# Kernel tuning notes

Measured on AMD Instinct MI355X. Metric: run time of the kernel, lower is better.

The kernel has to match this reference:

```python
import jax, jax.numpy as jnp
import numpy as np

B, S, D, H, DFF = 4, 2048, 1024, 16, 4096
DK = D // H
EPS = 1e-6


def setup_inputs() -> dict:
    key = jax.random.key(0)
    ks = jax.random.split(key, 8)
    s = 0.02
    return {
        "x": jax.random.normal(ks[0], (B, S, D), jnp.float32),
        "src_mask": jnp.ones((B, 1, 1, S), jnp.int32),
        "w_q": jax.random.normal(ks[1], (D, D), jnp.float32) * s,
        "w_k": jax.random.normal(ks[2], (D, D), jnp.float32) * s,
        "w_v": jax.random.normal(ks[3], (D, D), jnp.float32) * s,
        "w_o": jax.random.normal(ks[4], (D, D), jnp.float32) * s,
        "w1": jax.random.normal(ks[5], (DFF, D), jnp.float32) * s,
        "b1": jnp.zeros((DFF,), jnp.float32),
        "w2": jax.random.normal(ks[6], (D, DFF), jnp.float32) * s,
        "b2": jnp.zeros((D,), jnp.float32),
        "gamma1": jnp.ones((1,), jnp.float32),
        "beta1": jnp.zeros((1,), jnp.float32),
        "gamma2": jnp.ones((1,), jnp.float32),
        "beta2": jnp.zeros((1,), jnp.float32),
    }


def layernorm(x, gamma, beta):
    # matches torch source: unbiased std (ddof=1), eps added to std, scalar gamma/beta
    mean = jnp.mean(x, axis=-1, keepdims=True)
    std = jnp.std(x, axis=-1, keepdims=True, ddof=1)
    return gamma * (x - mean) / (std + EPS) + beta


def mha(x, w_q, w_k, w_v, w_o):
    # Linear(bias=False): y = x @ W.T
    q = (x @ w_q.T).reshape(B, S, H, DK).transpose(0, 2, 1, 3)  # [B,H,S,DK]
    k = (x @ w_k.T).reshape(B, S, H, DK).transpose(0, 2, 1, 3)
    v = (x @ w_v.T).reshape(B, S, H, DK).transpose(0, 2, 1, 3)
    scores = jnp.einsum('bhqd,bhkd->bhqk', q, k) / np.float32(np.sqrt(DK))
    # NOTE: source calls attention.masked_fill(...) without assigning the result,
    # so the mask has no effect; faithfully replicated (mask unused).
    attn = jax.nn.softmax(scores, axis=-1)
    ctx = jnp.einsum('bhqk,bhkd->bhqd', attn, v)  # [B,H,S,DK]
    ctx = ctx.transpose(0, 2, 1, 3).reshape(B, S, D)
    return ctx @ w_o.T


def ffn(x, w1, b1, w2, b2):
    return jax.nn.relu(x @ w1.T + b1) @ w2.T + b2


def reference(x, src_mask, w_q, w_k, w_v, w_o, w1, b1, w2, b2,
              gamma1, beta1, gamma2, beta2):
    # pre-norm residual blocks; dropout is identity in eval
    x = x + mha(layernorm(x, gamma1, beta1), w_q, w_k, w_v, w_o)
    x = x + ffn(layernorm(x, gamma2, beta2), w1, b1, w2, b2)
    return x
```

## Files before the change

kernel.cpp:

```cpp
#include <hip/hip_runtime.h>
#include <hip/hip_bf16.h>

#define DEV static __device__ __forceinline__

typedef unsigned short u16;
typedef float fp32x4 __attribute__((ext_vector_type(4)));
typedef short bf16x8 __attribute__((ext_vector_type(8)));
typedef short bf16x4 __attribute__((ext_vector_type(4)));

DEV float bf2f(u16 u) { return __uint_as_float(((unsigned)u) << 16); }
DEV u16 f2bf(float f) {
  unsigned x = __float_as_uint(f);
  x += 0x7fffu + ((x >> 16) & 1u);
  return (u16)(x >> 16);
}

DEV void gload_lds16(const void* g, void* l) {
  __builtin_amdgcn_global_load_lds(
      (__attribute__((address_space(1))) void*)(unsigned long long)g,
      (__attribute__((address_space(3))) void*)(unsigned int)(unsigned long long)l,
      16, 0, 0);
}

__global__ __launch_bounds__(256) void cvt_kernel(const float* __restrict__ in,
                                                  u16* __restrict__ out) {
  const int i = blockIdx.x * 256 + threadIdx.x;
  const fp32x4 v = ((const fp32x4*)in)[i];
  bf16x4 o;
#pragma unroll
  for (int j = 0; j < 4; j++) o[j] = (short)f2bf(v[j]);
  ((bf16x4*)out)[i] = o;
}

__global__ __launch_bounds__(256) void ln_kernel(const float* __restrict__ x,
                                                 u16* __restrict__ y,
                                                 const float* __restrict__ gamma,
                                                 const float* __restrict__ beta) {
  const int row = blockIdx.x;
  const int t = threadIdx.x;
  const fp32x4 v = ((const fp32x4*)(x + (size_t)row * 1024))[t];
  float s = v[0] + v[1] + v[2] + v[3];
  float ss = v[0] * v[0] + v[1] * v[1] + v[2] * v[2] + v[3] * v[3];
#pragma unroll
  for (int o = 32; o > 0; o >>= 1) {
    s += __shfl_down(s, o);
    ss += __shfl_down(ss, o);
  }
  __shared__ float rs[4], rss[4];
  const int w = t >> 6;
  if ((t & 63) == 0) { rs[w] = s; rss[w] = ss; }
  __syncthreads();
  const float S = rs[0] + rs[1] + rs[2] + rs[3];
  const float SS = rss[0] + rss[1] + rss[2] + rss[3];
  const float mean = S * (1.0f / 1024.0f);
  const float var = fmaxf((SS - 1024.0f * mean * mean) * (1.0f / 1023.0f), 0.0f);
  const float sc = gamma[0] / (sqrtf(var) + 1e-6f);
  const float be = beta[0];
  bf16x4 o;
#pragma unroll
  for (int j = 0; j < 4; j++) o[j] = (short)f2bf((v[j] - mean) * sc + be);
  ((bf16x4*)(y + (size_t)row * 1024))[t] = o;
}

template <int EPI>
__global__ __launch_bounds__(256, 2) void gemm_bt(
    const u16* __restrict__ A, const u16* __restrict__ W, u16* __restrict__ Cb,
    float* __restrict__ Cf, const float* __restrict__ bias,
    const float* __restrict__ resid, int M, int N, int K) {
  __shared__ u16 sA[128 * 32];
  __shared__ u16 sB[128 * 32];
  const int t = threadIdx.x;
  const int lane = t & 63;
  const int w = t >> 6;
  const int wr = (w >> 1) * 64;
  const int wc = (w & 1) * 64;
  const int lr = lane & 15;
  const int hi = lane >> 4;
  const int bx = blockIdx.x, by = blockIdx.y;

  const u16* gA = A + (size_t)(by * 128 + (t >> 2)) * K + (t & 3) * 8;
  const u16* gB = W + (size_t)(bx * 128 + (t >> 2)) * K + (t & 3) * 8;
  const size_t rstep = (size_t)64 * K;
  u16* lA = &sA[t * 8];
  u16* lB = &sB[t * 8];

  const fp32x4 zero4 = {0.f, 0.f, 0.f, 0.f};
  fp32x4 acc[4][4];
#pragma unroll
  for (int i = 0; i < 4; i++)
#pragma unroll
    for (int j = 0; j < 4; j++) acc[i][j] = zero4;

  for (int k0 = 0; k0 < K; k0 += 32) {
    gload_lds16(gA, lA);
    gload_lds16(gA + rstep, lA + 2048);
    gload_lds16(gB, lB);
    gload_lds16(gB + rstep, lB + 2048);
    gA += 32;
    gB += 32;
    __syncthreads();
    bf16x8 af[4], bfr[4];
#pragma unroll
    for (int i = 0; i < 4; i++)
      af[i] = *(const bf16x8*)&sA[(wr + i * 16 + lr) * 32 + hi * 8];
#pragma unroll
    for (int j = 0; j < 4; j++)
      bfr[j] = *(const bf16x8*)&sB[(wc + j * 16 + lr) * 32 + hi * 8];
#pragma unroll
    for (int i = 0; i < 4; i++)
#pragma unroll
      for (int j = 0; j < 4; j++)
        acc[i][j] =
            __builtin_amdgcn_mfma_f32_16x16x32_bf16(af[i], bfr[j], acc[i][j], 0, 0, 0);
    __syncthreads();
  }

  const int row0 = by * 128 + wr + hi * 4;
  const int col0 = bx * 128 + wc + lr;
  float bj[4] = {0.f, 0.f, 0.f, 0.f};
  if (EPI == 1 || EPI == 3) {
#pragma unroll
    for (int j = 0; j < 4; j++) bj[j] = bias[col0 + j * 16];
  }
#pragma unroll
  for (int i = 0; i < 4; i++) {
#pragma unroll
    for (int r = 0; r < 4; r++) {
      const size_t row = (size_t)(row0 + i * 16 + r);
#pragma unroll
      for (int j = 0; j < 4; j++) {
        const int col = col0 + j * 16;
        float v = acc[i][j][r];
        if (EPI == 1) v = fmaxf(v + bj[j], 0.f);
        if (EPI == 3) v += bj[j];
        if (EPI >= 2) {
          v += resid[row * N + col];
          Cf[row * N + col] = v;
        } else {
          Cb[row * N + col] = f2bf(v);
        }
      }
    }
  }
}

__global__ __launch_bounds__(256) void vtrans_kernel(const u16* __restrict__ V,
                                                     u16* __restrict__ VT) {
  const int st = blockIdx.x;
  const int h = blockIdx.y;
  const int b = blockIdx.z;
  const int t = threadIdx.x;
  const int r = t >> 2, c0 = (t & 3) * 16;
  __shared__ u16 sT[64][72];

  const u16* src = V + ((size_t)(b * 2048 + st * 64 + r)) * 1024 + h * 64 + c0;
  bf16x8 v0 = *(const bf16x8*)src;
  bf16x8 v1 = *(const bf16x8*)(src + 8);
  const int cb = c0 ^ ((r >> 4) << 4);
  *(bf16x8*)&sT[r][cb] = v0;
  *(bf16x8*)&sT[r][cb + 8] = v1;
  __syncthreads();

  const int dc = r ^ ((c0 >> 4) << 4);
  bf16x8 o0, o1;
#pragma unroll
  for (int i = 0; i < 8; i++) o0[i] = sT[c0 + i][dc];
#pragma unroll
  for (int i = 0; i < 8; i++) o1[i] = sT[c0 + 8 + i][dc];
  u16* dst = VT + ((size_t)((b * 16 + h) * 64 + r)) * 2048 + st * 64 + c0;
  *(bf16x8*)dst = o0;
  *(bf16x8*)(dst + 8) = o1;
}

__global__ __launch_bounds__(256, 2) void attn_kernel(const u16* __restrict__ Q,
                                                      const u16* __restrict__ K,
                                                      const u16* __restrict__ VT,
                                                      u16* __restrict__ O) {
  const int qt = blockIdx.x;
  const int h = blockIdx.y;
  const int b = blockIdx.z;
  const int t = threadIdx.x, lane = t & 63, w = t >> 6;
  const int lr = lane & 15, hi = lane >> 4;

  __shared__ u16 sK[64][72];
  __shared__ u16 sVT[64][72];
  __shared__ u16 sQP[64][72];

  const size_t base = ((size_t)b * 2048) * 1024 + (size_t)h * 64;
  const size_t vbase = (((size_t)b * 16 + h) * 64) * 2048;
  const int r = t >> 2, c0 = (t & 3) * 16;

  {
    const u16* src = Q + base + (size_t)(qt * 64 + r) * 1024 + c0;
    bf16x8 u0 = *(const bf16x8*)src;
    bf16x8 u1 = *(const bf16x8*)(src + 8);
#pragma unroll
    for (int i = 0; i < 8; i++) sQP[r][c0 + i] = f2bf(bf2f((u16)u0[i]) * 0.125f);
#pragma unroll
    for (int i = 0; i < 8; i++) sQP[r][c0 + 8 + i] = f2bf(bf2f((u16)u1[i]) * 0.125f);
  }
  __syncthreads();
  bf16x8 qreg0 = *(const bf16x8*)&sQP[w * 16 + lr][hi * 8];
  bf16x8 qreg1 = *(const bf16x8*)&sQP[w * 16 + lr][32 + hi * 8];

  bf16x8 kA, kB, vA, vB;
  {
    const u16* ks = K + base + (size_t)r * 1024 + c0;
    kA = *(const bf16x8*)ks;
    kB = *(const bf16x8*)(ks + 8);
    const u16* vs = VT + vbase + (size_t)r * 2048 + c0;
    vA = *(const bf16x8*)vs;
    vB = *(const bf16x8*)(vs + 8);
  }

  const fp32x4 zero4 = {0.f, 0.f, 0.f, 0.f};
  fp32x4 onT[4];
#pragma unroll
  for (int df = 0; df < 4; df++) onT[df] = zero4;
  float mrun = -1e30f, lrun = 0.f;

  for (int kt = 0; kt < 32; ++kt) {
    __syncthreads();
    *(bf16x8*)&sK[r][c0] = kA;
    *(bf16x8*)&sK[r][c0 + 8] = kB;
    *(bf16x8*)&sVT[r][c0] = vA;
    *(bf16x8*)&sVT[r][c0 + 8] = vB;
    __syncthreads();
    if (kt < 31) {
      const u16* kn = K + base + (size_t)((kt + 1) * 64 + r) * 1024 + c0;
      kA = *(const bf16x8*)kn;
      kB = *(const bf16x8*)(kn + 8);
      const u16* vn = VT + vbase + (size_t)r * 2048 + (kt + 1) * 64 + c0;
      vA = *(const bf16x8*)vn;
      vB = *(const bf16x8*)(vn + 8);
    }

    fp32x4 sc[4];
#pragma unroll
    for (int kk = 0; kk < 4; kk++) {
      fp32x4 a = zero4;
      bf16x8 kf0 = *(const bf16x8*)&sK[kk * 16 + lr][hi * 8];
      bf16x8 kf1 = *(const bf16x8*)&sK[kk * 16 + lr][32 + hi * 8];
      a = __builtin_amdgcn_mfma_f32_16x16x32_bf16(kf0, qreg0, a, 0, 0, 0);
      a = __builtin_amdgcn_mfma_f32_16x16x32_bf16(kf1, qreg1, a, 0, 0, 0);
      sc[kk] = a;
    }

    float mloc = -1e30f;
#pragma unroll
    for (int kk = 0; kk < 4; kk++)
#pragma unroll
      for (int rr = 0; rr < 4; rr++) mloc = fmaxf(mloc, sc[kk][rr]);
    mloc = fmaxf(mloc, __shfl_xor(mloc, 16));
    mloc = fmaxf(mloc, __shfl_xor(mloc, 32));
    const float mnew = fmaxf(mrun, mloc);
    const float alpha = __expf(mrun - mnew);
    float psum = 0.f;
#pragma unroll
    for (int kk = 0; kk < 4; kk++) {
      bf16x4 pv;
#pragma unroll
      for (int rr = 0; rr < 4; rr++) {
        const float p = __expf(sc[kk][rr] - mnew);
        psum += p;
        pv[rr] = (short)f2bf(p);
      }
      *(bf16x4*)&sQP[w * 16 + lr][kk * 16 + hi * 4] = pv;
    }
    psum += __shfl_xor(psum, 16);
    psum += __shfl_xor(psum, 32);
    lrun = lrun * alpha + psum;
    mrun = mnew;
#pragma unroll
    for (int df = 0; df < 4; df++) onT[df] *= alpha;

#pragma unroll
    for (int df = 0; df < 4; df++) {
#pragma unroll
      for (int ks = 0; ks < 2; ks++) {
        bf16x8 vf = *(const bf16x8*)&sVT[df * 16 + lr][ks * 32 + hi * 8];
        bf16x8 pf = *(const bf16x8*)&sQP[w * 16 + lr][ks * 32 + hi * 8];
        onT[df] = __builtin_amdgcn_mfma_f32_16x16x32_bf16(vf, pf, onT[df], 0, 0, 0);
      }
    }
  }

  const float invl = 1.0f / lrun;
  u16* dst = O + base + (size_t)(qt * 64 + w * 16 + lr) * 1024;
#pragma unroll
  for (int df = 0; df < 4; df++) {
    bf16x4 o4;
#pragma unroll
    for (int rr = 0; rr < 4; rr++) o4[rr] = (short)f2bf(onT[df][rr] * invl);
    *(bf16x4*)&dst[df * 16 + hi * 4] = o4;
  }
}

extern "C" void kernel_launch(void* const* d_in, const int* in_sizes, int n_in,
                              void* d_out, int out_size, void* d_ws, size_t ws_size,
                              hipStream_t stream) {
  const float* x = (const float*)d_in[0];
  const float* wq = (const float*)d_in[2];
  const float* wk = (const float*)d_in[3];
  const float* wv = (const float*)d_in[4];
  const float* wo = (const float*)d_in[5];
  const float* w1 = (const float*)d_in[6];
  const float* b1 = (const float*)d_in[7];
  const float* w2 = (const float*)d_in[8];
  const float* b2 = (const float*)d_in[9];
  const float* g1 = (const float*)d_in[10];
  const float* be1 = (const float*)d_in[11];
  const float* g2 = (const float*)d_in[12];
  const float* be2 = (const float*)d_in[13];
  float* out = (float*)d_out;

  const size_t MB = 1024ull * 1024ull;
  char* ws = (char*)d_ws;
  if (ws_size < 136 * MB) return;

  u16* wqb = (u16*)(ws + 0 * MB);
  u16* wkb = (u16*)(ws + 2 * MB);
  u16* wvb = (u16*)(ws + 4 * MB);
  u16* wob = (u16*)(ws + 6 * MB);
  u16* w1b = (u16*)(ws + 8 * MB);
  u16* w2b = (u16*)(ws + 16 * MB);
  u16* Qb = (u16*)(ws + 24 * MB);
  u16* Kb = (u16*)(ws + 40 * MB);
  u16* Vb = (u16*)(ws + 56 * MB);
  u16* Ctx = (u16*)(ws + 72 * MB);
  u16* Hb = (u16*)(ws + 24 * MB);
  u16* Yb = (u16*)(ws + 88 * MB);
  u16* VTb = (u16*)(ws + 88 * MB);
  float* X2 = (float*)(ws + 104 * MB);

  dim3 blk(256);

  cvt_kernel<<<1024, blk, 0, stream>>>(wq, wqb);
  cvt_kernel<<<1024, blk, 0, stream>>>(wk, wkb);
  cvt_kernel<<<1024, blk, 0, stream>>>(wv, wvb);
  cvt_kernel<<<1024, blk, 0, stream>>>(wo, wob);
  cvt_kernel<<<4096, blk, 0, stream>>>(w1, w1b);
  cvt_kernel<<<4096, blk, 0, stream>>>(w2, w2b);

  ln_kernel<<<8192, blk, 0, stream>>>(x, Yb, g1, be1);

  gemm_bt<0><<<dim3(8, 64), blk, 0, stream>>>(Yb, wqb, Qb, nullptr, nullptr, nullptr,
                                              8192, 1024, 1024);
  gemm_bt<0><<<dim3(8, 64), blk, 0, stream>>>(Yb, wkb, Kb, nullptr, nullptr, nullptr,
                                              8192, 1024, 1024);
  gemm_bt<0><<<dim3(8, 64), blk, 0, stream>>>(Yb, wvb, Vb, nullptr, nullptr, nullptr,
                                              8192, 1024, 1024);
  vtrans_kernel<<<dim3(32, 16, 4), blk, 0, stream>>>(Vb, VTb);

  attn_kernel<<<dim3(32, 16, 4), blk, 0, stream>>>(Qb, Kb, VTb, Ctx);

  gemm_bt<2><<<dim3(8, 64), blk, 0, stream>>>(Ctx, wob, nullptr, X2, nullptr, x, 8192,
                                              1024, 1024);

  ln_kernel<<<8192, blk, 0, stream>>>(X2, Yb, g2, be2);

  gemm_bt<1><<<dim3(32, 64), blk, 0, stream>>>(Yb, w1b, Hb, nullptr, b1, nullptr, 8192,
                                               4096, 1024);

  gemm_bt<3><<<dim3(8, 64), blk, 0, stream>>>(Hb, w2b, nullptr, out, b2, X2, 8192, 1024,
                                              4096);
}
```

Baseline: 499.7 us.

## Enlarge attention block to 128 queries with XOR-swizzled LDS and exp2 softmax

The attention kernel now runs 512 threads per block over 128 query rows, so each staged K/V tile is shared by twice as many query rows and K/V global traffic drops by half. Shared-memory indexing uses an XOR swizzle to avoid bank conflicts. The log2(e) factor is folded into the Q scale so softmax can use exp2f. Bf16 packing goes through v_cvt_pk_bf16_f32 instead of manual rounding. Launch bounds of (512, 8) may constrain registers, and the larger blocks halve the grid size.

```diff
diff --git a/kernel.cpp b/kernel.cpp
--- a/kernel.cpp
+++ b/kernel.cpp
@@ -13,6 +13,12 @@
   unsigned x = __float_as_uint(f);
   x += 0x7fffu + ((x >> 16) & 1u);
   return (u16)(x >> 16);
+}
+
+DEV unsigned cvt_pk_bf16(float a, float b) {
+  unsigned r;
+  asm("v_cvt_pk_bf16_f32 %0, %1, %2" : "=v"(r) : "v"(a), "v"(b));
+  return r;
 }
 
 DEV void gload_lds16(const void* g, void* l) {
@@ -172,7 +178,12 @@
   *(bf16x8*)(dst + 8) = o1;
 }
 
-__global__ __launch_bounds__(256, 2) void attn_kernel(const u16* __restrict__ Q,
+DEV u16* lp(u16* rowp, int row, int col) {
+  const int ch = col >> 3, sub = col & 7;
+  return rowp + (((ch ^ (row & 7)) << 3) + sub);
+}
+
+__global__ __launch_bounds__(512, 8) void attn_kernel(const u16* __restrict__ Q,
                                                       const u16* __restrict__ K,
                                                       const u16* __restrict__ VT,
                                                       u16* __restrict__ O) {
@@ -184,34 +195,36 @@
 
   __shared__ u16 sK[64][72];
   __shared__ u16 sVT[64][72];
-  __shared__ u16 sQP[64][72];
+  __shared__ u16 sQP[128][72];
 
   const size_t base = ((size_t)b * 2048) * 1024 + (size_t)h * 64;
   const size_t vbase = (((size_t)b * 16 + h) * 64) * 2048;
-  const int r = t >> 2, c0 = (t & 3) * 16;
 
   {
-    const u16* src = Q + base + (size_t)(qt * 64 + r) * 1024 + c0;
+    const int r = t >> 2, c0 = (t & 3) * 16;
+    const float qs = 0.125f * 1.44269504f;
+    const u16* src = Q + base + (size_t)(qt * 128 + r) * 1024 + c0;
     bf16x8 u0 = *(const bf16x8*)src;
     bf16x8 u1 = *(const bf16x8*)(src + 8);
-#pragma unroll
-    for (int i = 0; i < 8; i++) sQP[r][c0 + i] = f2bf(bf2f((u16)u0[i]) * 0.125f);
-#pragma unroll
-    for (int i = 0; i < 8; i++) sQP[r][c0 + 8 + i] = f2bf(bf2f((u16)u1[i]) * 0.125f);
+    union { unsigned u[4]; bf16x8 v; } q0, q1;
+#pragma unroll
+    for (int j = 0; j < 4; j++)
+      q0.u[j] = cvt_pk_bf16(bf2f((u16)u0[2 * j]) * qs, bf2f((u16)u0[2 * j + 1]) * qs);
+#pragma unroll
+    for (int j = 0; j < 4; j++)
+      q1.u[j] = cvt_pk_bf16(bf2f((u16)u1[2 * j]) * qs, bf2f((u16)u1[2 * j + 1]) * qs);
+    *(bf16x8*)lp(sQP[r], r, c0) = q0.v;
+    *(bf16x8*)lp(sQP[r], r, c0 + 8) = q1.v;
   }
   __syncthreads();
-  bf16x8 qreg0 = *(const bf16x8*)&sQP[w * 16 + lr][hi * 8];
-  bf16x8 qreg1 = *(const bf16x8*)&sQP[w * 16 + lr][32 + hi * 8];
-
-  bf16x8 kA, kB, vA, vB;
-  {
-    const u16* ks = K + base + (size_t)r * 1024 + c0;
-    kA = *(const bf16x8*)ks;
-    kB = *(const bf16x8*)(ks + 8);
-    const u16* vs = VT + vbase + (size_t)r * 2048 + c0;
-    vA = *(const bf16x8*)vs;
-    vB = *(const bf16x8*)(vs + 8);
-  }
+  const int qrow = w * 16 + lr;
+  bf16x8 qreg0 = *(const bf16x8*)lp(sQP[qrow], qrow, hi * 8);
+  bf16x8 qreg1 = *(const bf16x8*)lp(sQP[qrow], qrow, 32 + hi * 8);
+
+  const int rk = t >> 3, ck = (t & 7) * 8;
+  bf16x8 kA, vA;
+  kA = *(const bf16x8*)(K + base + (size_t)rk * 1024 + ck);
+  vA = *(const bf16x8*)(VT + vbase + (size_t)rk * 2048 + ck);
 
   const fp32x4 zero4 = {0.f, 0.f, 0.f, 0.f};
   fp32x4 onT[4];
@@ -221,26 +234,21 @@
 
   for (int kt = 0; kt < 32; ++kt) {
     __syncthreads();
-    *(bf16x8*)&sK[r][c0] = kA;
-    *(bf16x8*)&sK[r][c0 + 8] = kB;
-    *(bf16x8*)&sVT[r][c0] = vA;
-    *(bf16x8*)&sVT[r][c0 + 8] = vB;
+    *(bf16x8*)lp(sK[rk], rk, ck) = kA;
+    *(bf16x8*)lp(sVT[rk], rk, ck) = vA;
     __syncthreads();
     if (kt < 31) {
-      const u16* kn = K + base + (size_t)((kt + 1) * 64 + r) * 1024 + c0;
-      kA = *(const bf16x8*)kn;
-      kB = *(const bf16x8*)(kn + 8);
-      const u16* vn = VT + vbase + (size_t)r * 2048 + (kt + 1) * 64 + c0;
-      vA = *(const bf16x8*)vn;
-      vB = *(const bf16x8*)(vn + 8);
+      kA = *(const bf16x8*)(K + base + (size_t)((kt + 1) * 64 + rk) * 1024 + ck);
+      vA = *(const bf16x8*)(VT + vbase + (size_t)rk * 2048 + (kt + 1) * 64 + ck);
     }
 
     fp32x4 sc[4];
 #pragma unroll
     for (int kk = 0; kk < 4; kk++) {
       fp32x4 a = zero4;
-      bf16x8 kf0 = *(const bf16x8*)&sK[kk * 16 + lr][hi * 8];
-      bf16x8 kf1 = *(const bf16x8*)&sK[kk * 16 + lr][32 + hi * 8];
+      const int krow = kk * 16 + lr;
+      bf16x8 kf0 = *(const bf16x8*)lp(sK[krow], krow, hi * 8);
+      bf16x8 kf1 = *(const bf16x8*)lp(sK[krow], krow, 32 + hi * 8);
       a = __builtin_amdgcn_mfma_f32_16x16x32_bf16(kf0, qreg0, a, 0, 0, 0);
       a = __builtin_amdgcn_mfma_f32_16x16x32_bf16(kf1, qreg1, a, 0, 0, 0);
       sc[kk] = a;
@@ -254,18 +262,15 @@
     mloc = fmaxf(mloc, __shfl_xor(mloc, 16));
     mloc = fmaxf(mloc, __shfl_xor(mloc, 32));
     const float mnew = fmaxf(mrun, mloc);
-    const float alpha = __expf(mrun - mnew);
+    const float alpha = exp2f(mrun - mnew);
     float psum = 0.f;
 #pragma unroll
     for (int kk = 0; kk < 4; kk++) {
-      bf16x4 pv;
-#pragma unroll
-      for (int rr = 0; rr < 4; rr++) {
-        const float p = __expf(sc[kk][rr] - mnew);
-        psum += p;
-        pv[rr] = (short)f2bf(p);
-      }
-      *(bf16x4*)&sQP[w * 16 + lr][kk * 16 + hi * 4] = pv;
+      float p0 = exp2f(sc[kk][0] - mnew), p1 = exp2f(sc[kk][1] - mnew);
+      float p2 = exp2f(sc[kk][2] - mnew), p3 = exp2f(sc[kk][3] - mnew);
+      psum += (p0 + p1) + (p2 + p3);
+      uint2 pk = {cvt_pk_bf16(p0, p1), cvt_pk_bf16(p2, p3)};
+      *(uint2*)lp(sQP[qrow], qrow, kk * 16 + hi * 4) = pk;
     }
     psum += __shfl_xor(psum, 16);
     psum += __shfl_xor(psum, 32);
@@ -276,23 +281,23 @@
 
 #pragma unroll
     for (int df = 0; df < 4; df++) {
+      const int vrow = df * 16 + lr;
 #pragma unroll
       for (int ks = 0; ks < 2; ks++) {
-        bf16x8 vf = *(const bf16x8*)&sVT[df * 16 + lr][ks * 32 + hi * 8];
-        bf16x8 pf = *(const bf16x8*)&sQP[w * 16 + lr][ks * 32 + hi * 8];
+        bf16x8 vf = *(const bf16x8*)lp(sVT[vrow], vrow, ks * 32 + hi * 8);
+        bf16x8 pf = *(const bf16x8*)lp(sQP[qrow], qrow, ks * 32 + hi * 8);
         onT[df] = __builtin_amdgcn_mfma_f32_16x16x32_bf16(vf, pf, onT[df], 0, 0, 0);
       }
     }
   }
 
   const float invl = 1.0f / lrun;
-  u16* dst = O + base + (size_t)(qt * 64 + w * 16 + lr) * 1024;
+  u16* dst = O + base + (size_t)(qt * 128 + qrow) * 1024;
 #pragma unroll
   for (int df = 0; df < 4; df++) {
-    bf16x4 o4;
-#pragma unroll
-    for (int rr = 0; rr < 4; rr++) o4[rr] = (short)f2bf(onT[df][rr] * invl);
-    *(bf16x4*)&dst[df * 16 + hi * 4] = o4;
+    uint2 o2 = {cvt_pk_bf16(onT[df][0] * invl, onT[df][1] * invl),
+                cvt_pk_bf16(onT[df][2] * invl, onT[df][3] * invl)};
+    *(uint2*)&dst[df * 16 + hi * 4] = o2;
   }
 }
 
@@ -352,7 +357,7 @@
                                               8192, 1024, 1024);
   vtrans_kernel<<<dim3(32, 16, 4), blk, 0, stream>>>(Vb, VTb);
 
-  attn_kernel<<<dim3(32, 16, 4), blk, 0, stream>>>(Qb, Kb, VTb, Ctx);
+  attn_kernel<<<dim3(16, 16, 4), dim3(512), 0, stream>>>(Qb, Kb, VTb, Ctx);
 
   gemm_bt<2><<<dim3(8, 64), blk, 0, stream>>>(Ctx, wob, nullptr, X2, nullptr, x, 8192,
                                               1024, 1024);
```

Result: slower. 562.1 us (+12.5%).
